# Performance work log

Measured on AMD Instinct MI355X. Metric: run time of the kernel, lower is better.

Reference implementation:

```python
import jax, jax.numpy as jnp
import numpy as np

B, SQ, FDIM = 32, 196, 2048
L, EDIM, H = 1000, 1024, 16
DH = EDIM // H  # 64


def setup_inputs() -> dict:
    key = jax.random.key(0)
    ks = jax.random.split(key, 10)
    s = lambda fan_in: 1.0 / np.sqrt(fan_in)
    return {
        "features": jax.random.normal(ks[0], (B, SQ, FDIM), jnp.float32),
        "label_embeddings": jax.random.normal(ks[1], (L, EDIM), jnp.float32),
        "Wq": jax.random.normal(ks[2], (EDIM, FDIM), jnp.float32) * s(FDIM),
        "bq": jax.random.normal(ks[3], (EDIM,), jnp.float32) * s(FDIM),
        "Wk": jax.random.normal(ks[4], (EDIM, EDIM), jnp.float32) * s(EDIM),
        "bk": jax.random.normal(ks[5], (EDIM,), jnp.float32) * s(EDIM),
        "Wv": jax.random.normal(ks[6], (EDIM, EDIM), jnp.float32) * s(EDIM),
        "bv": jax.random.normal(ks[7], (EDIM,), jnp.float32) * s(EDIM),
        "Wo": jax.random.normal(ks[8], (EDIM, EDIM), jnp.float32) * s(EDIM),
        "bo": jax.random.normal(ks[9], (EDIM,), jnp.float32) * s(EDIM),
    }


def reference(features, label_embeddings, Wq, bq, Wk, bk, Wv, bv, Wo, bo):
    # Q projection: [B, Sq, E] -> [B, Sq, H, Dh]
    q = (jnp.einsum("bsf,ef->bse", features, Wq) + bq).reshape(B, SQ, H, DH)
    # K/V projections on the shared label table: [L, E] -> [L, H, Dh]
    k = (label_embeddings @ Wk.T + bk).reshape(L, H, DH)
    v = (label_embeddings @ Wv.T + bv).reshape(L, H, DH)
    # scores: [B, H, Sq, L]
    scores = jnp.einsum("bqhd,lhd->bhql", q, k) / jnp.sqrt(jnp.float32(DH))
    attn = jax.nn.softmax(scores, axis=-1)
    # attention output: [B, Sq, H, Dh] -> [B, Sq, E]
    ctx = jnp.einsum("bhql,lhd->bqhd", attn, v).reshape(B, SQ, EDIM)
    return jnp.einsum("bse,oe->bso", ctx, Wo) + bo
```

## Files before the change

kernel.cpp:

```cpp
#include <hip/hip_runtime.h>
#include <hip/hip_bf16.h>
#include <stdint.h>
#include <math.h>

constexpr int BB   = 32;
constexpr int SQ   = 196;
constexpr int FDIM = 2048;
constexpr int LL   = 1000;
constexpr int EDIM = 1024;
constexpr int HH   = 16;
constexpr int BSQ  = BB * SQ;

typedef unsigned short u16;
typedef unsigned int   u32;
typedef __attribute__((ext_vector_type(4)))  float f32x4;
typedef __attribute__((ext_vector_type(16))) float f32x16;
typedef __attribute__((ext_vector_type(8)))  short bf16x8;
typedef __attribute__((ext_vector_type(2)))  int   i32x2;

#define DEV __device__ __forceinline__

DEV u16 f2bf(float f) {
  unsigned u = __float_as_uint(f);
  unsigned r = 0x7FFFu + ((u >> 16) & 1u);
  return (u16)((u + r) >> 16);
}

DEV u32 pack2bf(float a, float b) {
  __hip_bfloat162 h = __float22bfloat162_rn(float2{a, b});
  return *reinterpret_cast<const u32*>(&h);
}

#if __has_builtin(__builtin_amdgcn_exp2f)
#define EXP2F(x) __builtin_amdgcn_exp2f(x)
#else
#define EXP2F(x) exp2f(x)
#endif

DEV f32x16 zero16() {
  f32x16 v;
#pragma unroll
  for (int i = 0; i < 16; ++i) v[i] = 0.f;
  return v;
}

#if __has_builtin(__builtin_amdgcn_permlane32_swap)
DEV void half_swap(u32& a, u32& b, int ) {
  i32x2 r = __builtin_amdgcn_permlane32_swap((int)a, (int)b, false, false);
  a = (u32)r[0]; b = (u32)r[1];
}
#else
DEV void half_swap(u32& a, u32& b, int hi) {
  const u32 sa = __shfl_xor(a, 32), sb = __shfl_xor(b, 32);
  const u32 na = hi ? sb : a;
  const u32 nb = hi ? b : sa;
  a = na; b = nb;
}
#endif

#define GLDS16(g, l) __builtin_amdgcn_global_load_lds(                         \
    (const __attribute__((address_space(1))) void*)(g),                       \
    (__attribute__((address_space(3))) void*)(l), 16, 0, 0)

DEV int xcd_chunk(int bid, int cpx) { return (bid & 7) * cpx + (bid >> 3); }

constexpr int C_N0 = BSQ * FDIM / 4;
constexpr int C_N1 = C_N0 + EDIM * FDIM / 4;
constexpr int C_N2 = C_N1 + EDIM * EDIM / 4;
constexpr int C_N3 = C_N2 + EDIM * EDIM / 4;
constexpr int C_N4 = C_N3 + EDIM * EDIM / 4;
constexpr int C_N5 = C_N4 + LL * EDIM / 4;

__global__ void cvt_all(const float* __restrict__ f,  const float* __restrict__ wq,
                        const float* __restrict__ wk, const float* __restrict__ wv,
                        const float* __restrict__ wo, const float* __restrict__ lab,
                        u16* df, u16* dwq, u16* dwk, u16* dwv, u16* dwo, u16* dlab) {
  int i = blockIdx.x * blockDim.x + threadIdx.x;
  const int st = gridDim.x * blockDim.x;
  for (; i < C_N5; i += st) {
    const float* s; u16* d; int j;
    if (i < C_N0)      { s = f;   d = df;   j = i; }
    else if (i < C_N1) { s = wq;  d = dwq;  j = i - C_N0; }
    else if (i < C_N2) { s = wk;  d = dwk;  j = i - C_N1; }
    else if (i < C_N3) { s = wv;  d = dwv;  j = i - C_N2; }
    else if (i < C_N4) { s = wo;  d = dwo;  j = i - C_N3; }
    else               { s = lab; d = dlab; j = i - C_N4; }
    float4 v = reinterpret_cast<const float4*>(s)[j];
    ushort4 o;
    o.x = f2bf(v.x); o.y = f2bf(v.y); o.z = f2bf(v.z); o.w = f2bf(v.w);
    reinterpret_cast<ushort4*>(d)[j] = o;
  }
}

template<bool OUT_BF16>
DEV void gemm_body(u16* sA, u16* sB, int bid,
                   const u16* __restrict__ A,
                   const u16* B1, const float* bias1, void* C1,
                   const u16* B2, const float* bias2, void* C2,
                   int M, int K, int ntn, int ntiles_n1, float scale, int c2t) {
  const int tn  = bid % ntn;
  const int tm  = bid / ntn;

  const u16* Bp; const float* biasp; void* Cp; int tnl; bool tw;
  if (tn < ntiles_n1) { Bp = B1; biasp = bias1; Cp = C1; tnl = tn; tw = false; }
  else { Bp = B2; biasp = bias2; Cp = C2; tnl = tn - ntiles_n1; tw = (c2t != 0); }

  const int lane = threadIdx.x & 63;
  const int wid  = threadIdx.x >> 6;
  const int wr   = wid >> 1, wc = wid & 1;
  const int lr   = lane & 15, lg = lane >> 4;

  f32x4 acc[4][4];
#pragma unroll
  for (int m = 0; m < 4; ++m)
#pragma unroll
    for (int n = 0; n < 4; ++n) acc[m][n] = (f32x4){0.f, 0.f, 0.f, 0.f};

  for (int k0 = 0; k0 < K; k0 += 64) {
#pragma unroll
    for (int i = 0; i < 4; ++i) {
      const int chunk = wid * 4 + i;
      const int row   = chunk * 8 + (lane >> 3);
      const int col   = (lane & 7) * 8;
      int ga = tm * 128 + row; ga = ga < M ? ga : M - 1;
      GLDS16(A + (size_t)ga * K + k0 + col, &sA[chunk * 512]);
      const int gb = tnl * 128 + row;
      GLDS16(Bp + (size_t)gb * K + k0 + col, &sB[chunk * 512]);
    }
    asm volatile("s_waitcnt vmcnt(0)" ::: "memory");
    __syncthreads();
#pragma unroll
    for (int ks = 0; ks < 2; ++ks) {
      bf16x8 af[4], bfr[4];
#pragma unroll
      for (int m = 0; m < 4; ++m)
        af[m] = *reinterpret_cast<const bf16x8*>(&sA[(wr * 64 + m * 16 + lr) * 64 + ks * 32 + lg * 8]);
#pragma unroll
      for (int n = 0; n < 4; ++n)
        bfr[n] = *reinterpret_cast<const bf16x8*>(&sB[(wc * 64 + n * 16 + lr) * 64 + ks * 32 + lg * 8]);
#pragma unroll
      for (int m = 0; m < 4; ++m)
#pragma unroll
        for (int n = 0; n < 4; ++n)
          acc[m][n] = __builtin_amdgcn_mfma_f32_16x16x32_bf16(af[m], bfr[n], acc[m][n], 0, 0, 0);
    }
    __syncthreads();
  }

#pragma unroll
  for (int n = 0; n < 4; ++n) {
    const int c  = tnl * 128 + wc * 64 + n * 16 + lr;
    const float bv = biasp[c];
#pragma unroll
    for (int m = 0; m < 4; ++m) {
#pragma unroll
      for (int r = 0; r < 4; ++r) {
        const int rr = tm * 128 + wr * 64 + m * 16 + lg * 4 + r;
        const float v = (acc[m][n][r] + bv) * scale;
        if (OUT_BF16) {
          if (tw)
            ((u16*)Cp)[(size_t)c * 1024 + rr] = (rr < M) ? f2bf(v) : (u16)0;
          else if (rr < M)
            ((u16*)Cp)[(size_t)rr * 1024 + c] = f2bf(v);
        } else if (rr < M)
          ((float*)Cp)[(size_t)rr * 1024 + c] = v;
      }
    }
  }
}

__global__ __launch_bounds__(256)
void gemm_proj_fused(const u16* fA, const u16* wq, const float* bq, u16* qo,
                     const u16* lA, const u16* wk, const float* bk, u16* ko,
                     const u16* wv, const float* bv, u16* vto,
                     float qscale) {
  __shared__ __attribute__((aligned(16))) u16 sA[128 * 64];
  __shared__ __attribute__((aligned(16))) u16 sB[128 * 64];
  const int bid = blockIdx.x;
  if (bid < 392) {
    const int nb = xcd_chunk(bid, 49);
    gemm_body<true>(sA, sB, nb, fA, wq, bq, qo,
                    nullptr, nullptr, nullptr, BSQ, FDIM, 8, 8, qscale, 0);
  } else {
    int nb = xcd_chunk(bid - 392, 16);
    nb = (nb % 8) * 16 + (nb / 8);
    gemm_body<true>(sA, sB, nb, lA, wk, bk, ko,
                    wv, bv, vto, LL, EDIM, 16, 8, 1.0f, 1);
  }
}

__global__ __launch_bounds__(256)
void gemm_oproj(const u16* A, const u16* B, const float* bias, float* C) {
  __shared__ __attribute__((aligned(16))) u16 sA[128 * 64];
  __shared__ __attribute__((aligned(16))) u16 sB[128 * 64];
  const int nb = xcd_chunk(blockIdx.x, 49);
  gemm_body<false>(sA, sB, nb, A, B, bias, C,
                   nullptr, nullptr, nullptr, BSQ, EDIM, 8, 8, 1.0f, 0);
}

__global__ __launch_bounds__(256, 2)
void attn_kernel(const u16* __restrict__ Q, const u16* __restrict__ Kb,
                 const u16* __restrict__ VT, u16* __restrict__ ctx) {
  const int wg = xcd_chunk(blockIdx.x, 98);
  const int h = wg / 49, qb = wg % 49;
  __shared__ __attribute__((aligned(16))) u16 sm[16384];

  const int t    = threadIdx.x;
  const int lane = t & 63;
  const int wid  = t >> 6;
  const int l31  = lane & 31, hi = lane >> 5;

  const int qrow = qb * 128 + wid * 32 + l31;
  const u16* qp = Q + (size_t)qrow * EDIM + h * 64;
  bf16x8 qf[4];
#pragma unroll
  for (int ks = 0; ks < 4; ++ks)
    qf[ks] = *reinterpret_cast<const bf16x8*>(qp + ks * 16 + hi * 8);

  f32x16 ctxa[2]; ctxa[0] = zero16(); ctxa[1] = zero16();
  float lsum = 0.f;

  auto stage = [&](int buf, int l0s) {
#pragma unroll
    for (int i = 0; i < 2; ++i) {
      const int chunk = wid * 2 + i;
      const int row   = chunk * 8 + (lane >> 3);
      const int sl    = (lane & 7) ^ (row & 7);
      int lk = l0s + row; if (lk > LL - 1) lk = LL - 1;
      GLDS16(Kb + (size_t)lk * EDIM + h * 64 + sl * 8, sm + buf * 4096 + chunk * 512);
      GLDS16(VT + (size_t)(h * 64 + row) * 1024 + l0s + sl * 8, sm + 8192 + buf * 4096 + chunk * 512);
    }
  };
  auto frag = [&](const u16* base, int row, int slot) -> bf16x8 {
    return *reinterpret_cast<const bf16x8*>(base + row * 64 + ((slot ^ (row & 7)) * 8));
  };

  constexpr int NT = (LL + 63) / 64;
  stage(0, 0);
  asm volatile("s_waitcnt vmcnt(0)" ::: "memory");
  __syncthreads();

  for (int it = 0; it < NT; ++it) {
    const int l0  = it * 64;
    const int cur = it & 1;
    if (it + 1 < NT) stage(cur ^ 1, l0 + 64);

    const u16* sKb = sm + cur * 4096;
    const u16* sVb = sm + 8192 + cur * 4096;

    f32x16 st[2]; st[0] = zero16(); st[1] = zero16();
    __builtin_amdgcn_s_setprio(1);
#pragma unroll
    for (int ks = 0; ks < 4; ++ks) {
#pragma unroll
      for (int jt = 0; jt < 2; ++jt) {
        bf16x8 kf = frag(sKb, jt * 32 + l31, 2 * ks + hi);
        st[jt] = __builtin_amdgcn_mfma_f32_32x32x16_bf16(kf, qf[ks], st[jt], 0, 0, 0);
      }
    }
    __builtin_amdgcn_s_setprio(0);

    u32 pk[2][4][2];
    auto softmax_pack = [&](bool tail) {
#pragma unroll
      for (int jt = 0; jt < 2; ++jt) {
#pragma unroll
        for (int g = 0; g < 4; ++g) {
          float p[4];
#pragma unroll
          for (int j = 0; j < 4; ++j) {
            float e = EXP2F(st[jt][g * 4 + j]);
            if (tail) {
              const int kg = l0 + jt * 32 + j + 8 * g + 4 * hi;
              if (kg >= LL) e = 0.f;
            }
            p[j] = e;
            lsum += e;
          }
          pk[jt][g][0] = pack2bf(p[0], p[1]);
          pk[jt][g][1] = pack2bf(p[2], p[3]);
        }
      }
    };
    if (l0 + 64 <= LL) softmax_pack(false); else softmax_pack(true);

    __builtin_amdgcn_s_setprio(1);
#pragma unroll
    for (int ksl = 0; ksl < 4; ++ksl) {
      const int jt = ksl >> 1, e2 = ksl & 1;
      u32 x0 = pk[jt][2 * e2 + 0][0], y0 = pk[jt][2 * e2 + 1][0];
      u32 x1 = pk[jt][2 * e2 + 0][1], y1 = pk[jt][2 * e2 + 1][1];
      half_swap(x0, y0, hi);
      half_swap(x1, y1, hi);
      union { u32 d[4]; bf16x8 v; } pf;
      pf.d[0] = x0; pf.d[1] = x1; pf.d[2] = y0; pf.d[3] = y1;
#pragma unroll
      for (int dt = 0; dt < 2; ++dt) {
        bf16x8 vf = frag(sVb, dt * 32 + l31, 2 * ksl + hi);
        ctxa[dt] = __builtin_amdgcn_mfma_f32_32x32x16_bf16(vf, pf.v, ctxa[dt], 0, 0, 0);
      }
    }
    __builtin_amdgcn_s_setprio(0);

    asm volatile("s_waitcnt vmcnt(0)" ::: "memory");
    __syncthreads();
  }

  float ltot = lsum + __shfl_xor(lsum, 32);
  const float inv = 1.0f / ltot;

  u16* tb = sm;
  const int q = wid * 32 + l31;
#pragma unroll
  for (int dt = 0; dt < 2; ++dt) {
#pragma unroll
    for (int g = 0; g < 4; ++g) {
      u32 w0 = pack2bf(ctxa[dt][g * 4 + 0] * inv, ctxa[dt][g * 4 + 1] * inv);
      u32 w1 = pack2bf(ctxa[dt][g * 4 + 2] * inv, ctxa[dt][g * 4 + 3] * inv);
      const int d2   = dt * 64 + g * 16 + hi * 8;
      const int byte = q * 128 + (d2 ^ ((q & 7) << 4));
      *reinterpret_cast<u32*>(reinterpret_cast<char*>(tb) + byte)     = w0;
      *reinterpret_cast<u32*>(reinterpret_cast<char*>(tb) + byte + 4) = w1;
    }
  }
  __syncthreads();
#pragma unroll
  for (int pass = 0; pass < 4; ++pass) {
    const int row  = pass * 32 + (t >> 3);
    const int srow = qb * 128 + row;
    const int cb = ((t & 7) * 16) ^ ((row & 7) << 4);
    uint4 val = *reinterpret_cast<const uint4*>(reinterpret_cast<const char*>(tb) + row * 128 + cb);
    *reinterpret_cast<uint4*>(ctx + (size_t)srow * EDIM + h * 64 + (t & 7) * 8) = val;
  }
}

extern "C" void kernel_launch(void* const* d_in, const int* in_sizes, int n_in,
                              void* d_out, int out_size, void* d_ws, size_t ws_size,
                              hipStream_t stream) {
  const float* features = (const float*)d_in[0];
  const float* labels   = (const float*)d_in[1];
  const float* Wq = (const float*)d_in[2];
  const float* bq = (const float*)d_in[3];
  const float* Wk = (const float*)d_in[4];
  const float* bk = (const float*)d_in[5];
  const float* Wv = (const float*)d_in[6];
  const float* bv = (const float*)d_in[7];
  const float* Wo = (const float*)d_in[8];
  const float* bo = (const float*)d_in[9];
  float* out = (float*)d_out;

  u16* f_bf   = (u16*)d_ws;
  u16* wq_bf  = f_bf   + (size_t)BSQ  * FDIM;
  u16* wk_bf  = wq_bf  + (size_t)EDIM * FDIM;
  u16* wv_bf  = wk_bf  + (size_t)EDIM * EDIM;
  u16* wo_bf  = wv_bf  + (size_t)EDIM * EDIM;
  u16* lab_bf = wo_bf  + (size_t)EDIM * EDIM;
  u16* q_bf   = lab_bf + (size_t)LL   * EDIM;
  u16* k_bf   = q_bf   + (size_t)BSQ  * EDIM;
  u16* vt_bf  = k_bf   + (size_t)LL   * EDIM;
  u16* ctx_bf = vt_bf  + (size_t)1024 * 1024;

  cvt_all<<<2048, 256, 0, stream>>>(features, Wq, Wk, Wv, Wo, labels,
                                    f_bf, wq_bf, wk_bf, wv_bf, wo_bf, lab_bf);

  const float qscale = 0.125f * 1.4426950408889634f;
  gemm_proj_fused<<<49 * 8 + 8 * 16, 256, 0, stream>>>(
      f_bf, wq_bf, bq, q_bf, lab_bf, wk_bf, bk, k_bf, wv_bf, bv, vt_bf, qscale);

  attn_kernel<<<784, 256, 0, stream>>>(q_bf, k_bf, vt_bf, ctx_bf);

  gemm_oproj<<<49 * 8, 256, 0, stream>>>(ctx_bf, wo_bf, bo, out);
}
```

Before: 159.6 us.

## Double-buffer LDS tiles in GEMM body to overlap global loads with MFMA

The shared GEMM routine now uses two LDS buffers for the A and B tiles. It issues the direct-to-LDS loads for tile k+1 before computing on tile k, and one barrier per iteration replaces the explicit vmcnt wait plus two barriers. This is meant to hide global-memory latency behind the matrix-core work in the Q/K/V projection and output projection kernels. It doubles LDS use per block to 64KB, which may lower occupancy. It also drops the explicit vmcnt(0) wait, so correctness depends on the barrier lowering waiting for the outstanding LDS-DMA loads.

```diff
diff --git a/kernel.cpp b/kernel.cpp
--- a/kernel.cpp
+++ b/kernel.cpp
@@ -93,7 +93,7 @@
 }
 
 template<bool OUT_BF16>
-DEV void gemm_body(u16* sA, u16* sB, int bid,
+DEV void gemm_body(u16* sAb, u16* sBb, int bid,
                    const u16* __restrict__ A,
                    const u16* B1, const float* bias1, void* C1,
                    const u16* B2, const float* bias2, void* C2,
@@ -110,25 +110,37 @@
   const int wr   = wid >> 1, wc = wid & 1;
   const int lr   = lane & 15, lg = lane >> 4;
 
+  const int schunk = wid * 4;
+  const int srow   = (lane >> 3);
+  const int scol   = (lane & 7) * 8;
+
   f32x4 acc[4][4];
 #pragma unroll
   for (int m = 0; m < 4; ++m)
 #pragma unroll
     for (int n = 0; n < 4; ++n) acc[m][n] = (f32x4){0.f, 0.f, 0.f, 0.f};
 
-  for (int k0 = 0; k0 < K; k0 += 64) {
+  auto stage = [&](int buf, int k0) {
 #pragma unroll
     for (int i = 0; i < 4; ++i) {
-      const int chunk = wid * 4 + i;
-      const int row   = chunk * 8 + (lane >> 3);
-      const int col   = (lane & 7) * 8;
+      const int chunk = schunk + i;
+      const int row   = chunk * 8 + srow;
       int ga = tm * 128 + row; ga = ga < M ? ga : M - 1;
-      GLDS16(A + (size_t)ga * K + k0 + col, &sA[chunk * 512]);
+      GLDS16(A + (size_t)ga * K + k0 + scol, sAb + buf * 8192 + chunk * 512);
       const int gb = tnl * 128 + row;
-      GLDS16(Bp + (size_t)gb * K + k0 + col, &sB[chunk * 512]);
-    }
-    asm volatile("s_waitcnt vmcnt(0)" ::: "memory");
-    __syncthreads();
+      GLDS16(Bp + (size_t)gb * K + k0 + scol, sBb + buf * 8192 + chunk * 512);
+    }
+  };
+
+  const int NK = K >> 6;
+  stage(0, 0);
+  __syncthreads();
+
+  int bufc = 0;
+  for (int t = 0; t < NK; ++t) {
+    if (t + 1 < NK) stage(bufc ^ 1, (t + 1) << 6);
+    const u16* sA = sAb + bufc * 8192;
+    const u16* sB = sBb + bufc * 8192;
 #pragma unroll
     for (int ks = 0; ks < 2; ++ks) {
       bf16x8 af[4], bfr[4];
@@ -145,6 +157,7 @@
           acc[m][n] = __builtin_amdgcn_mfma_f32_16x16x32_bf16(af[m], bfr[n], acc[m][n], 0, 0, 0);
     }
     __syncthreads();
+    bufc ^= 1;
   }
 
 #pragma unroll
@@ -174,27 +187,27 @@
                      const u16* lA, const u16* wk, const float* bk, u16* ko,
                      const u16* wv, const float* bv, u16* vto,
                      float qscale) {
-  __shared__ __attribute__((aligned(16))) u16 sA[128 * 64];
-  __shared__ __attribute__((aligned(16))) u16 sB[128 * 64];
+  __shared__ __attribute__((aligned(16))) u16 sAb[2 * 128 * 64];
+  __shared__ __attribute__((aligned(16))) u16 sBb[2 * 128 * 64];
   const int bid = blockIdx.x;
   if (bid < 392) {
     const int nb = xcd_chunk(bid, 49);
-    gemm_body<true>(sA, sB, nb, fA, wq, bq, qo,
+    gemm_body<true>(sAb, sBb, nb, fA, wq, bq, qo,
                     nullptr, nullptr, nullptr, BSQ, FDIM, 8, 8, qscale, 0);
   } else {
     int nb = xcd_chunk(bid - 392, 16);
     nb = (nb % 8) * 16 + (nb / 8);
-    gemm_body<true>(sA, sB, nb, lA, wk, bk, ko,
+    gemm_body<true>(sAb, sBb, nb, lA, wk, bk, ko,
                     wv, bv, vto, LL, EDIM, 16, 8, 1.0f, 1);
   }
 }
 
 __global__ __launch_bounds__(256)
 void gemm_oproj(const u16* A, const u16* B, const float* bias, float* C) {
-  __shared__ __attribute__((aligned(16))) u16 sA[128 * 64];
-  __shared__ __attribute__((aligned(16))) u16 sB[128 * 64];
+  __shared__ __attribute__((aligned(16))) u16 sAb[2 * 128 * 64];
+  __shared__ __attribute__((aligned(16))) u16 sBb[2 * 128 * 64];
   const int nb = xcd_chunk(blockIdx.x, 49);
-  gemm_body<false>(sA, sB, nb, A, B, bias, C,
+  gemm_body<false>(sAb, sBb, nb, A, B, bias, C,
                    nullptr, nullptr, nullptr, BSQ, EDIM, 8, 8, 1.0f, 0);
 }
 
```

After: 162.6 us. No clear change (+1.8%).

## Fuse fp32 feature conversion into Q-projection GEMM and retile output projection

Applied to the files above, without the earlier changes.

The separate bf16 conversion pass over the large features tensor is removed. The Q-projection GEMM now loads fp32 features directly, converts them in registers and writes bf16 to shared memory, which avoids one full write and re-read of a large intermediate. The output projection gets its own kernel with 64x128 tiles and 784 blocks for better occupancy and load balance. The trade-off is that the Q GEMM's A loads become synchronous register loads instead of async global-to-LDS copies, and each of the 8 N-tiles re-reads the fp32 features at twice the bytes.

```diff
diff --git a/kernel.cpp b/kernel.cpp
--- a/kernel.cpp
+++ b/kernel.cpp
@@ -64,27 +64,25 @@
 
 DEV int xcd_chunk(int bid, int cpx) { return (bid & 7) * cpx + (bid >> 3); }
 
-constexpr int C_N0 = BSQ * FDIM / 4;
-constexpr int C_N1 = C_N0 + EDIM * FDIM / 4;
+constexpr int C_N0 = EDIM * FDIM / 4;
+constexpr int C_N1 = C_N0 + EDIM * EDIM / 4;
 constexpr int C_N2 = C_N1 + EDIM * EDIM / 4;
 constexpr int C_N3 = C_N2 + EDIM * EDIM / 4;
-constexpr int C_N4 = C_N3 + EDIM * EDIM / 4;
-constexpr int C_N5 = C_N4 + LL * EDIM / 4;
-
-__global__ void cvt_all(const float* __restrict__ f,  const float* __restrict__ wq,
+constexpr int C_N4 = C_N3 + LL * EDIM / 4;
+
+__global__ void cvt_all(const float* __restrict__ wq,
                         const float* __restrict__ wk, const float* __restrict__ wv,
                         const float* __restrict__ wo, const float* __restrict__ lab,
-                        u16* df, u16* dwq, u16* dwk, u16* dwv, u16* dwo, u16* dlab) {
+                        u16* dwq, u16* dwk, u16* dwv, u16* dwo, u16* dlab) {
   int i = blockIdx.x * blockDim.x + threadIdx.x;
   const int st = gridDim.x * blockDim.x;
-  for (; i < C_N5; i += st) {
+  for (; i < C_N4; i += st) {
     const float* s; u16* d; int j;
-    if (i < C_N0)      { s = f;   d = df;   j = i; }
-    else if (i < C_N1) { s = wq;  d = dwq;  j = i - C_N0; }
-    else if (i < C_N2) { s = wk;  d = dwk;  j = i - C_N1; }
-    else if (i < C_N3) { s = wv;  d = dwv;  j = i - C_N2; }
-    else if (i < C_N4) { s = wo;  d = dwo;  j = i - C_N3; }
-    else               { s = lab; d = dlab; j = i - C_N4; }
+    if (i < C_N0)      { s = wq;  d = dwq;  j = i; }
+    else if (i < C_N1) { s = wk;  d = dwk;  j = i - C_N0; }
+    else if (i < C_N2) { s = wv;  d = dwv;  j = i - C_N1; }
+    else if (i < C_N3) { s = wo;  d = dwo;  j = i - C_N2; }
+    else               { s = lab; d = dlab; j = i - C_N3; }
     float4 v = reinterpret_cast<const float4*>(s)[j];
     ushort4 o;
     o.x = f2bf(v.x); o.y = f2bf(v.y); o.z = f2bf(v.z); o.w = f2bf(v.w);
@@ -92,9 +90,9 @@
   }
 }
 
-template<bool OUT_BF16>
+template<bool OUT_BF16, bool A_F32>
 DEV void gemm_body(u16* sA, u16* sB, int bid,
-                   const u16* __restrict__ A,
+                   const void* Ap_,
                    const u16* B1, const float* bias1, void* C1,
                    const u16* B2, const float* bias2, void* C2,
                    int M, int K, int ntn, int ntiles_n1, float scale, int c2t) {
@@ -117,15 +115,36 @@
     for (int n = 0; n < 4; ++n) acc[m][n] = (f32x4){0.f, 0.f, 0.f, 0.f};
 
   for (int k0 = 0; k0 < K; k0 += 64) {
+    if (A_F32) {
+      const float* A32 = (const float*)Ap_;
+#pragma unroll
+      for (int i = 0; i < 4; ++i) {
+        const int chunk = wid * 4 + i;
+        const int row   = chunk * 8 + (lane >> 3);
+        const size_t off = (size_t)(tm * 128 + row) * K + k0 + (lane & 7) * 8;
+        const float4 f0 = *reinterpret_cast<const float4*>(A32 + off);
+        const float4 f1 = *reinterpret_cast<const float4*>(A32 + off + 4);
+        uint4 w;
+        w.x = pack2bf(f0.x, f0.y); w.y = pack2bf(f0.z, f0.w);
+        w.z = pack2bf(f1.x, f1.y); w.w = pack2bf(f1.z, f1.w);
+        *reinterpret_cast<uint4*>(&sA[chunk * 512 + lane * 8]) = w;
+      }
+    } else {
+      const u16* Abf = (const u16*)Ap_;
+#pragma unroll
+      for (int i = 0; i < 4; ++i) {
+        const int chunk = wid * 4 + i;
+        const int row   = chunk * 8 + (lane >> 3);
+        int ga = tm * 128 + row; ga = ga < M ? ga : M - 1;
+        GLDS16(Abf + (size_t)ga * K + k0 + (lane & 7) * 8, &sA[chunk * 512]);
+      }
+    }
 #pragma unroll
     for (int i = 0; i < 4; ++i) {
       const int chunk = wid * 4 + i;
       const int row   = chunk * 8 + (lane >> 3);
-      const int col   = (lane & 7) * 8;
-      int ga = tm * 128 + row; ga = ga < M ? ga : M - 1;
-      GLDS16(A + (size_t)ga * K + k0 + col, &sA[chunk * 512]);
       const int gb = tnl * 128 + row;
-      GLDS16(Bp + (size_t)gb * K + k0 + col, &sB[chunk * 512]);
+      GLDS16(Bp + (size_t)gb * K + k0 + (lane & 7) * 8, &sB[chunk * 512]);
     }
     asm volatile("s_waitcnt vmcnt(0)" ::: "memory");
     __syncthreads();
@@ -170,7 +189,7 @@
 }
 
 __global__ __launch_bounds__(256)
-void gemm_proj_fused(const u16* fA, const u16* wq, const float* bq, u16* qo,
+void gemm_proj_fused(const float* fA, const u16* wq, const float* bq, u16* qo,
                      const u16* lA, const u16* wk, const float* bk, u16* ko,
                      const u16* wv, const float* bv, u16* vto,
                      float qscale) {
@@ -179,23 +198,80 @@
   const int bid = blockIdx.x;
   if (bid < 392) {
     const int nb = xcd_chunk(bid, 49);
-    gemm_body<true>(sA, sB, nb, fA, wq, bq, qo,
-                    nullptr, nullptr, nullptr, BSQ, FDIM, 8, 8, qscale, 0);
+    gemm_body<true, true>(sA, sB, nb, fA, wq, bq, qo,
+                          nullptr, nullptr, nullptr, BSQ, FDIM, 8, 8, qscale, 0);
   } else {
     int nb = xcd_chunk(bid - 392, 16);
     nb = (nb % 8) * 16 + (nb / 8);
-    gemm_body<true>(sA, sB, nb, lA, wk, bk, ko,
-                    wv, bv, vto, LL, EDIM, 16, 8, 1.0f, 1);
+    gemm_body<true, false>(sA, sB, nb, lA, wk, bk, ko,
+                           wv, bv, vto, LL, EDIM, 16, 8, 1.0f, 1);
   }
 }
 
 __global__ __launch_bounds__(256)
-void gemm_oproj(const u16* A, const u16* B, const float* bias, float* C) {
-  __shared__ __attribute__((aligned(16))) u16 sA[128 * 64];
+void gemm_oproj(const u16* __restrict__ A, const u16* __restrict__ B,
+                const float* __restrict__ bias, float* __restrict__ C) {
+  __shared__ __attribute__((aligned(16))) u16 sA[64 * 64];
   __shared__ __attribute__((aligned(16))) u16 sB[128 * 64];
-  const int nb = xcd_chunk(blockIdx.x, 49);
-  gemm_body<false>(sA, sB, nb, A, B, bias, C,
-                   nullptr, nullptr, nullptr, BSQ, EDIM, 8, 8, 1.0f, 0);
+  const int nb = xcd_chunk(blockIdx.x, 98);
+  const int tn = nb % 8, tm = nb / 8;
+
+  const int lane = threadIdx.x & 63;
+  const int wid  = threadIdx.x >> 6;
+  const int lr = lane & 15, lg = lane >> 4;
+
+  f32x4 acc[4][2];
+#pragma unroll
+  for (int m = 0; m < 4; ++m)
+#pragma unroll
+    for (int n = 0; n < 2; ++n) acc[m][n] = (f32x4){0.f, 0.f, 0.f, 0.f};
+
+  for (int k0 = 0; k0 < EDIM; k0 += 64) {
+#pragma unroll
+    for (int i = 0; i < 2; ++i) {
+      const int chunk = wid * 2 + i;
+      const int row = chunk * 8 + (lane >> 3);
+      GLDS16(A + (size_t)(tm * 64 + row) * 1024 + k0 + (lane & 7) * 8, &sA[chunk * 512]);
+    }
+#pragma unroll
+    for (int i = 0; i < 4; ++i) {
+      const int chunk = wid * 4 + i;
+      const int row = chunk * 8 + (lane >> 3);
+      GLDS16(B + (size_t)(tn * 128 + row) * 1024 + k0 + (lane & 7) * 8, &sB[chunk * 512]);
+    }
+    asm volatile("s_waitcnt vmcnt(0)" ::: "memory");
+    __syncthreads();
+#pragma unroll
+    for (int ks = 0; ks < 2; ++ks) {
+      bf16x8 af[4], bfr[2];
+#pragma unroll
+      for (int m = 0; m < 4; ++m)
+        af[m] = *reinterpret_cast<const bf16x8*>(&sA[(m * 16 + lr) * 64 + ks * 32 + lg * 8]);
+#pragma unroll
+      for (int n = 0; n < 2; ++n)
+        bfr[n] = *reinterpret_cast<const bf16x8*>(&sB[(wid * 32 + n * 16 + lr) * 64 + ks * 32 + lg * 8]);
+#pragma unroll
+      for (int m = 0; m < 4; ++m)
+#pragma unroll
+        for (int n = 0; n < 2; ++n)
+          acc[m][n] = __builtin_amdgcn_mfma_f32_16x16x32_bf16(af[m], bfr[n], acc[m][n], 0, 0, 0);
+    }
+    __syncthreads();
+  }
+
+#pragma unroll
+  for (int n = 0; n < 2; ++n) {
+    const int c = tn * 128 + wid * 32 + n * 16 + lr;
+    const float bv = bias[c];
+#pragma unroll
+    for (int m = 0; m < 4; ++m) {
+#pragma unroll
+      for (int r = 0; r < 4; ++r) {
+        const int rr = tm * 64 + m * 16 + lg * 4 + r;
+        C[(size_t)rr * 1024 + c] = acc[m][n][r] + bv;
+      }
+    }
+  }
 }
 
 __global__ __launch_bounds__(256, 2)
@@ -349,8 +425,7 @@
   const float* bo = (const float*)d_in[9];
   float* out = (float*)d_out;
 
-  u16* f_bf   = (u16*)d_ws;
-  u16* wq_bf  = f_bf   + (size_t)BSQ  * FDIM;
+  u16* wq_bf  = (u16*)d_ws;
   u16* wk_bf  = wq_bf  + (size_t)EDIM * FDIM;
   u16* wv_bf  = wk_bf  + (size_t)EDIM * EDIM;
   u16* wo_bf  = wv_bf  + (size_t)EDIM * EDIM;
@@ -360,14 +435,14 @@
   u16* vt_bf  = k_bf   + (size_t)LL   * EDIM;
   u16* ctx_bf = vt_bf  + (size_t)1024 * 1024;
 
-  cvt_all<<<2048, 256, 0, stream>>>(features, Wq, Wk, Wv, Wo, labels,
-                                    f_bf, wq_bf, wk_bf, wv_bf, wo_bf, lab_bf);
+  cvt_all<<<1024, 256, 0, stream>>>(Wq, Wk, Wv, Wo, labels,
+                                    wq_bf, wk_bf, wv_bf, wo_bf, lab_bf);
 
   const float qscale = 0.125f * 1.4426950408889634f;
   gemm_proj_fused<<<49 * 8 + 8 * 16, 256, 0, stream>>>(
-      f_bf, wq_bf, bq, q_bf, lab_bf, wk_bf, bk, k_bf, wv_bf, bv, vt_bf, qscale);
+      features, wq_bf, bq, q_bf, lab_bf, wk_bf, bk, k_bf, wv_bf, bv, vt_bf, qscale);
 
   attn_kernel<<<784, 256, 0, stream>>>(q_bf, k_bf, vt_bf, ctx_bf);
 
-  gemm_oproj<<<49 * 8, 256, 0, stream>>>(ctx_bf, wo_bf, bo, out);
-}
+  gemm_oproj<<<784, 256, 0, stream>>>(ctx_bf, wo_bf, bo, out);
+}
```

Measured after the change: 154.8 us. 3.1% less time.
